# Optimization experiments

Hardware: AMD Instinct MI355X
Metric: run time of the kernel (lower is better)

## Reference

```python
import jax, jax.numpy as jnp
from jax import lax
import numpy as np

B, T, IN, H, OUT = 1024, 512, 64, 128, 2
BN_EPS = 1e-5


def _gru_layer(x, w_ih, w_hh, b_ih, b_hh):
    # x: [B, T, F]; w_ih: [3H, F]; w_hh: [3H, H]; gate order = (r, z, n) as in PyTorch
    Bb = x.shape[0]
    Hh = w_hh.shape[1]
    xg = jnp.einsum('btf,gf->btg', x, w_ih) + b_ih  # precompute input gates [B, T, 3H]

    def step(h, xg_t):
        hg = h @ w_hh.T + b_hh                       # [B, 3H]
        xr, xz, xn = jnp.split(xg_t, 3, axis=-1)
        hr, hz, hn = jnp.split(hg, 3, axis=-1)
        r = jax.nn.sigmoid(xr + hr)
        z = jax.nn.sigmoid(xz + hz)
        n = jnp.tanh(xn + r * hn)
        h_new = (1.0 - z) * n + z * h
        return h_new, h_new

    h0 = jnp.zeros((Bb, Hh), dtype=x.dtype)
    _, ys = lax.scan(step, h0, jnp.swapaxes(xg, 0, 1))  # scan over time
    return jnp.swapaxes(ys, 0, 1)                        # [B, T, H]


def setup_inputs() -> dict:
    key = jax.random.key(0)
    ks = jax.random.split(key, 16)
    s_in = 1.0 / np.sqrt(H)  # PyTorch GRU init scale
    d = {
        'x': jax.random.normal(ks[0], (B, T, IN), dtype=jnp.float32),
        'w_ih0': jax.random.uniform(ks[1], (3 * H, IN), minval=-s_in, maxval=s_in),
        'w_hh0': jax.random.uniform(ks[2], (3 * H, H), minval=-s_in, maxval=s_in),
        'b_ih0': jax.random.uniform(ks[3], (3 * H,), minval=-s_in, maxval=s_in),
        'b_hh0': jax.random.uniform(ks[4], (3 * H,), minval=-s_in, maxval=s_in),
        'w_ih1': jax.random.uniform(ks[5], (3 * H, H), minval=-s_in, maxval=s_in),
        'w_hh1': jax.random.uniform(ks[6], (3 * H, H), minval=-s_in, maxval=s_in),
        'b_ih1': jax.random.uniform(ks[7], (3 * H,), minval=-s_in, maxval=s_in),
        'b_hh1': jax.random.uniform(ks[8], (3 * H,), minval=-s_in, maxval=s_in),
        'fc1_w': jax.random.normal(ks[9], (H // 2, H)) * 0.05,
        'fc1_b': jnp.zeros((H // 2,)),
        'fc2_w': jax.random.normal(ks[10], (OUT, H // 2)) * 0.05,
        'fc2_b': jnp.zeros((OUT,)),
        'bn_gamma': jnp.ones((H // 2,)),
        'bn_beta': jnp.zeros((H // 2,)),
        'bn_mean': jnp.zeros((H // 2,)),
        'bn_var': jnp.ones((H // 2,)),
    }
    return d


def reference(x, w_ih0, w_hh0, b_ih0, b_hh0, w_ih1, w_hh1, b_ih1, b_hh1,
              fc1_w, fc1_b, fc2_w, fc2_b, bn_gamma, bn_beta, bn_mean, bn_var):
    h1 = _gru_layer(x, w_ih0, w_hh0, b_ih0, b_hh0)   # [B, T, H]
    h2 = _gru_layer(h1, w_ih1, w_hh1, b_ih1, b_hh1)  # [B, T, H]
    out = h2[:, -1, :]                                # last timestep [B, H]
    # dropout = identity (eval mode)
    out = jax.nn.relu(out @ fc1_w.T + fc1_b)          # [B, H/2]
    out = (out - bn_mean) * jax.lax.rsqrt(bn_var + BN_EPS) * bn_gamma + bn_beta
    out = out @ fc2_w.T + fc2_b                       # [B, 2]
    return out
```

## Files before the change

kernel.cpp:

```cpp
#include <hip/hip_runtime.h>
#include <hip/hip_bf16.h>

namespace {

typedef _Float16 h16;
typedef _Float16 f16x8 __attribute__((ext_vector_type(8)));
typedef _Float16 f16x4 __attribute__((ext_vector_type(4)));
typedef _Float16 f16x2 __attribute__((ext_vector_type(2)));
typedef float    f32x4 __attribute__((ext_vector_type(4)));

constexpr int T_SEQ = 512;
constexpr int B_SZ  = 1024;
constexpr int H_DIM = 128;
constexpr int ROWS  = 16;
constexpr int NT    = 512;
constexpr int KSH   = 4;
constexpr int KSX0  = 2;
constexpr int KSX1  = 4;
constexpr int ROWP0 = 192 + 8;
constexpr int ROWP1 = 256 + 8;

__global__ __launch_bounds__(NT, 1)
void gru2(const float* __restrict__ x,
          const float* __restrict__ w_ih0,
          const float* __restrict__ w_hh0,
          const float* __restrict__ b_ih0, const float* __restrict__ b_hh0,
          const float* __restrict__ w_ih1,
          const float* __restrict__ w_hh1,
          const float* __restrict__ b_ih1, const float* __restrict__ b_hh1,
          float* __restrict__ h2out)
{
  __shared__ __align__(16) h16 hx0[2][ROWS][ROWP0];
  __shared__ __align__(16) h16 hx1[2][ROWS][ROWP1];

  const int tid = threadIdx.x;
  const int wv  = tid >> 6;
  const int ln  = tid & 63;
  const int q   = ln >> 4;
  const int lr  = ln & 15;
  const int r0  = blockIdx.x * ROWS;
  const int j0  = wv * 16 + q * 4;

  auto ldw = [](const float* pw) {
    const float4 v0 = *(const float4*)(pw);
    const float4 v1 = *(const float4*)(pw + 4);
    f16x8 f;
    f[0]=(h16)v0.x; f[1]=(h16)v0.y; f[2]=(h16)v0.z; f[3]=(h16)v0.w;
    f[4]=(h16)v1.x; f[5]=(h16)v1.y; f[6]=(h16)v1.z; f[7]=(h16)v1.w;
    return f;
  };

  f16x8 wA0[3][KSH], wB0[3][KSX0], wA1[3][KSH], wB1[3][KSX1];
  #pragma unroll
  for (int p = 0; p < 3; ++p) {
    const int g = p * H_DIM + wv * 16 + lr;
    #pragma unroll
    for (int ks = 0; ks < KSH; ++ks) {
      wA0[p][ks] = ldw(w_hh0 + (size_t)g * H_DIM + ks * 32 + q * 8);
      wA1[p][ks] = ldw(w_hh1 + (size_t)g * H_DIM + ks * 32 + q * 8);
    }
    #pragma unroll
    for (int ks = 0; ks < KSX0; ++ks)
      wB0[p][ks] = ldw(w_ih0 + (size_t)g * 64 + ks * 32 + q * 8);
    #pragma unroll
    for (int ks = 0; ks < KSX1; ++ks)
      wB1[p][ks] = ldw(w_ih1 + (size_t)g * H_DIM + ks * 32 + q * 8);
  }

  f32x4 bR0, bZ0, bNx0, bNh0, bR1, bZ1, bNx1, bNh1;
  {
    auto mkb = [&](const float* bi, const float* bh,
                   f32x4& bR, f32x4& bZ, f32x4& bNx, f32x4& bNh) {
      const float4 ir  = *(const float4*)&bi[j0];
      const float4 hr  = *(const float4*)&bh[j0];
      const float4 iz  = *(const float4*)&bi[H_DIM + j0];
      const float4 hz  = *(const float4*)&bh[H_DIM + j0];
      const float4 in_ = *(const float4*)&bi[2 * H_DIM + j0];
      const float4 hn  = *(const float4*)&bh[2 * H_DIM + j0];
      bR[0]=ir.x+hr.x; bR[1]=ir.y+hr.y; bR[2]=ir.z+hr.z; bR[3]=ir.w+hr.w;
      bZ[0]=iz.x+hz.x; bZ[1]=iz.y+hz.y; bZ[2]=iz.z+hz.z; bZ[3]=iz.w+hz.w;
      bNx[0]=in_.x; bNx[1]=in_.y; bNx[2]=in_.z; bNx[3]=in_.w;
      bNh[0]=hn.x;  bNh[1]=hn.y;  bNh[2]=hn.z;  bNh[3]=hn.w;
    };
    mkb(b_ih0, b_hh0, bR0, bZ0, bNx0, bNh0);
    mkb(b_ih1, b_hh1, bR1, bZ1, bNx1, bNh1);
  }

  const int sr = tid >> 5;
  const int si = tid & 31;

  {
    f16x4 z; z[0]=z[1]=z[2]=z[3] = (h16)0.f;
    *(f16x4*)&hx0[0][tid >> 5][(tid & 31) * 4] = z;
    *(f16x4*)&hx1[1][tid >> 5][(tid & 31) * 4] = z;
  }
  {
    const float2 v = *(const float2*)(x + ((size_t)(r0 + sr) * T_SEQ + 0) * 64 + si * 2);
    f16x2 s0; s0[0] = (h16)v.x; s0[1] = (h16)v.y;
    *(f16x2*)&hx0[0][sr][H_DIM + si * 2] = s0;
  }
  f16x2 sA, sB;
  {
    const float2 v = *(const float2*)(x + ((size_t)(r0 + sr) * T_SEQ + 1) * 64 + si * 2);
    sA[0] = (h16)v.x; sA[1] = (h16)v.y;
  }
  f16x4 h_old0, h_old1;
  h_old0[0]=h_old0[1]=h_old0[2]=h_old0[3] = (h16)0.f;
  h_old1 = h_old0;
  __syncthreads();

  auto gates = [&](const f32x4& aR, const f32x4& aZ, const f32x4& aNx, const f32x4& aNh,
                   f16x4& h_old, float* hnv) -> f16x4 {
    f16x4 nv4;
    #pragma unroll
    for (int i = 0; i < 4; ++i) {
      const float rg = __builtin_amdgcn_rcpf(1.f + __expf(-aR[i]));
      const float zg = __builtin_amdgcn_rcpf(1.f + __expf(-aZ[i]));
      const float na = aNx[i] + rg * aNh[i];
      const float e2 = __expf(2.f * na);
      const float ng = 1.f - 2.f * __builtin_amdgcn_rcpf(e2 + 1.f);
      const float ho = (float)h_old[i];
      const float hn = ng + zg * (ho - ng);
      hnv[i] = hn;
      nv4[i] = (h16)hn;
    }
    h_old = nv4;
    return nv4;
  };

  auto l0_step = [&](int g, int cur, f16x2& s_use, f16x2& s_load) {
    f16x8 bh[KSH], bx[KSX0];
    #pragma unroll
    for (int ks = 0; ks < KSH; ++ks)
      bh[ks] = *(const f16x8*)&hx0[cur][lr][ks * 32 + q * 8];
    #pragma unroll
    for (int ks = 0; ks < KSX0; ++ks)
      bx[ks] = *(const f16x8*)&hx0[cur][lr][H_DIM + ks * 32 + q * 8];

    {
      const int tt = (g + 2 < T_SEQ) ? g + 2 : T_SEQ - 1;
      const float2 v = *(const float2*)(x + ((size_t)(r0 + sr) * T_SEQ + tt) * 64 + si * 2);
      s_load[0] = (h16)v.x; s_load[1] = (h16)v.y;
    }

    f32x4 aR = bR0, aZ = bZ0, aNh = bNh0, aNx = bNx0;
    #pragma unroll
    for (int ks = 0; ks < KSH; ++ks) {
      aR  = __builtin_amdgcn_mfma_f32_16x16x32_f16(wA0[0][ks], bh[ks], aR, 0, 0, 0);
      aZ  = __builtin_amdgcn_mfma_f32_16x16x32_f16(wA0[1][ks], bh[ks], aZ, 0, 0, 0);
      aNh = __builtin_amdgcn_mfma_f32_16x16x32_f16(wA0[2][ks], bh[ks], aNh, 0, 0, 0);
    }
    #pragma unroll
    for (int ks = 0; ks < KSX0; ++ks) {
      aR  = __builtin_amdgcn_mfma_f32_16x16x32_f16(wB0[0][ks], bx[ks], aR, 0, 0, 0);
      aZ  = __builtin_amdgcn_mfma_f32_16x16x32_f16(wB0[1][ks], bx[ks], aZ, 0, 0, 0);
      aNx = __builtin_amdgcn_mfma_f32_16x16x32_f16(wB0[2][ks], bx[ks], aNx, 0, 0, 0);
    }

    float hnv[4];
    const f16x4 nv4 = gates(aR, aZ, aNx, aNh, h_old0, hnv);
    *(f16x4*)&hx0[cur ^ 1][lr][j0] = nv4;
    *(f16x4*)&hx1[cur ^ 1][lr][H_DIM + j0] = nv4;
    *(f16x2*)&hx0[cur ^ 1][sr][H_DIM + si * 2] = s_use;
  };

  auto l1_step = [&](int cur, bool final_store) {
    f16x8 bh[KSH], bx[KSX1];
    #pragma unroll
    for (int ks = 0; ks < KSH; ++ks)
      bh[ks] = *(const f16x8*)&hx1[cur][lr][ks * 32 + q * 8];
    #pragma unroll
    for (int ks = 0; ks < KSX1; ++ks)
      bx[ks] = *(const f16x8*)&hx1[cur][lr][H_DIM + ks * 32 + q * 8];

    f32x4 aR = bR1, aZ = bZ1, aNh = bNh1, aNx = bNx1;
    #pragma unroll
    for (int ks = 0; ks < KSH; ++ks) {
      aR  = __builtin_amdgcn_mfma_f32_16x16x32_f16(wA1[0][ks], bh[ks], aR, 0, 0, 0);
      aZ  = __builtin_amdgcn_mfma_f32_16x16x32_f16(wA1[1][ks], bh[ks], aZ, 0, 0, 0);
      aNh = __builtin_amdgcn_mfma_f32_16x16x32_f16(wA1[2][ks], bh[ks], aNh, 0, 0, 0);
    }
    #pragma unroll
    for (int ks = 0; ks < KSX1; ++ks) {
      aR  = __builtin_amdgcn_mfma_f32_16x16x32_f16(wB1[0][ks], bx[ks], aR, 0, 0, 0);
      aZ  = __builtin_amdgcn_mfma_f32_16x16x32_f16(wB1[1][ks], bx[ks], aZ, 0, 0, 0);
      aNx = __builtin_amdgcn_mfma_f32_16x16x32_f16(wB1[2][ks], bx[ks], aNx, 0, 0, 0);
    }

    float hnv[4];
    const f16x4 nv4 = gates(aR, aZ, aNx, aNh, h_old1, hnv);
    *(f16x4*)&hx1[cur ^ 1][lr][j0] = nv4;
    if (final_store)
      *(float4*)&h2out[(size_t)(r0 + lr) * H_DIM + j0] =
          make_float4(hnv[0], hnv[1], hnv[2], hnv[3]);
  };

  l0_step(0, 0, sA, sB);
  __syncthreads();

  #pragma unroll 1
  for (int k = 0; k < (T_SEQ - 2) / 2; ++k) {
    l0_step(2 * k + 1, 1, sB, sA);
    l1_step(1, false);
    __syncthreads();
    l0_step(2 * k + 2, 0, sA, sB);
    l1_step(0, false);
    __syncthreads();
  }
  l0_step(T_SEQ - 1, 1, sB, sA);
  l1_step(1, false);
  __syncthreads();
  l1_step(0, true);
}

__global__ __launch_bounds__(64)
void head_kernel(const float* __restrict__ h2,
                 const float* __restrict__ fc1_w, const float* __restrict__ fc1_b,
                 const float* __restrict__ fc2_w, const float* __restrict__ fc2_b,
                 const float* __restrict__ gamma, const float* __restrict__ beta,
                 const float* __restrict__ mean,  const float* __restrict__ var,
                 float* __restrict__ out)
{
  const int row = blockIdx.x;
  const int j   = threadIdx.x;
  __shared__ __align__(16) float hrow[H_DIM];
  __shared__ __align__(16) float act[64];

  hrow[j]      = h2[(size_t)row * H_DIM + j];
  hrow[64 + j] = h2[(size_t)row * H_DIM + 64 + j];
  __syncthreads();

  float s = fc1_b[j];
  const float4* wr = reinterpret_cast<const float4*>(fc1_w + (size_t)j * H_DIM);
  #pragma unroll
  for (int k4 = 0; k4 < H_DIM / 4; ++k4) {
    const float4 w = wr[k4];
    const float4 h = reinterpret_cast<const float4*>(hrow)[k4];
    s += w.x * h.x + w.y * h.y + w.z * h.z + w.w * h.w;
  }
  s = fmaxf(s, 0.f);
  s = (s - mean[j]) * rsqrtf(var[j] + 1e-5f) * gamma[j] + beta[j];
  act[j] = s;
  __syncthreads();

  if (j < 2) {
    float o = fc2_b[j];
    #pragma unroll
    for (int k = 0; k < 64; ++k) o += fc2_w[(size_t)j * 64 + k] * act[k];
    out[(size_t)row * 2 + j] = o;
  }
}

}

extern "C" void kernel_launch(void* const* d_in, const int* in_sizes, int n_in,
                              void* d_out, int out_size, void* d_ws, size_t ws_size,
                              hipStream_t stream) {
  const float* x     = (const float*)d_in[0];
  const float* w_ih0 = (const float*)d_in[1];
  const float* w_hh0 = (const float*)d_in[2];
  const float* b_ih0 = (const float*)d_in[3];
  const float* b_hh0 = (const float*)d_in[4];
  const float* w_ih1 = (const float*)d_in[5];
  const float* w_hh1 = (const float*)d_in[6];
  const float* b_ih1 = (const float*)d_in[7];
  const float* b_hh1 = (const float*)d_in[8];
  const float* fc1_w = (const float*)d_in[9];
  const float* fc1_b = (const float*)d_in[10];
  const float* fc2_w = (const float*)d_in[11];
  const float* fc2_b = (const float*)d_in[12];
  const float* gamma = (const float*)d_in[13];
  const float* beta  = (const float*)d_in[14];
  const float* mean  = (const float*)d_in[15];
  const float* var   = (const float*)d_in[16];
  float* out = (float*)d_out;

  const size_t h2_bytes = (size_t)B_SZ * H_DIM * sizeof(float);
  if (ws_size < h2_bytes) return;
  float* h2 = (float*)d_ws;

  gru2<<<dim3(B_SZ / ROWS), dim3(NT), 0, stream>>>(
      x, w_ih0, w_hh0, b_ih0, b_hh0, w_ih1, w_hh1, b_ih1, b_hh1, h2);
  head_kernel<<<dim3(B_SZ), dim3(64), 0, stream>>>(
      h2, fc1_w, fc1_b, fc2_w, fc2_b, gamma, beta, mean, var, out);
}
```

Baseline: 702.0 us.

## Reuse layer-0 hidden fragments for layer-1 input gates and swizzle LDS layout

Layer 1's input-gate projection is now computed inside the layer-0 step, reusing the h1 fragments already loaded for layer 0's recurrent matmul, instead of separately reading h1 from a concatenated layer-1 buffer. The LDS buffers are repacked into a fragment-major slot layout so each lane reads one contiguous 16-byte chunk (ln-indexed), which is meant to avoid bank conflicts and padding. The x staging switches to 8-wide vector loads done by two waves. This lowers the LDS reads and writes per step but holds the layer-1 input gates in registers across the barrier, raising register pressure.

```diff
diff --git a/kernel.cpp b/kernel.cpp
--- a/kernel.cpp
+++ b/kernel.cpp
@@ -6,7 +6,6 @@
 typedef _Float16 h16;
 typedef _Float16 f16x8 __attribute__((ext_vector_type(8)));
 typedef _Float16 f16x4 __attribute__((ext_vector_type(4)));
-typedef _Float16 f16x2 __attribute__((ext_vector_type(2)));
 typedef float    f32x4 __attribute__((ext_vector_type(4)));
 
 constexpr int T_SEQ = 512;
@@ -14,11 +13,13 @@
 constexpr int H_DIM = 128;
 constexpr int ROWS  = 16;
 constexpr int NT    = 512;
-constexpr int KSH   = 4;
-constexpr int KSX0  = 2;
-constexpr int KSX1  = 4;
-constexpr int ROWP0 = 192 + 8;
-constexpr int ROWP1 = 256 + 8;
+constexpr int CH    = 4;
+constexpr int CX    = 2;
+
+constexpr int FH1 = 0;
+constexpr int FX  = 2 * CH * 64;
+constexpr int FH2 = FX + 2 * CX * 64;
+constexpr int NSLOT = FH2 + 2 * CH * 64;
 
 __global__ __launch_bounds__(NT, 1)
 void gru2(const float* __restrict__ x,
@@ -30,8 +31,7 @@
           const float* __restrict__ b_ih1, const float* __restrict__ b_hh1,
           float* __restrict__ h2out)
 {
-  __shared__ __align__(16) h16 hx0[2][ROWS][ROWP0];
-  __shared__ __align__(16) h16 hx1[2][ROWS][ROWP1];
+  __shared__ __align__(16) h16 lds[NSLOT * 8];
 
   const int tid = threadIdx.x;
   const int wv  = tid >> 6;
@@ -41,6 +41,9 @@
   const int r0  = blockIdx.x * ROWS;
   const int j0  = wv * 16 + q * 4;
 
+  const int slotH = (wv >> 1) * 64 + ((wv & 1) * 2 + (q >> 1)) * 16 + lr;
+  const int e0    = (q & 1) * 4;
+
   auto ldw = [](const float* pw) {
     const float4 v0 = *(const float4*)(pw);
     const float4 v1 = *(const float4*)(pw + 4);
@@ -50,21 +53,19 @@
     return f;
   };
 
-  f16x8 wA0[3][KSH], wB0[3][KSX0], wA1[3][KSH], wB1[3][KSX1];
+  f16x8 wA0[3][CH], wB0[3][CX], wI1[3][CH], wA1[3][CH];
   #pragma unroll
   for (int p = 0; p < 3; ++p) {
     const int g = p * H_DIM + wv * 16 + lr;
     #pragma unroll
-    for (int ks = 0; ks < KSH; ++ks) {
+    for (int ks = 0; ks < CH; ++ks) {
       wA0[p][ks] = ldw(w_hh0 + (size_t)g * H_DIM + ks * 32 + q * 8);
+      wI1[p][ks] = ldw(w_ih1 + (size_t)g * H_DIM + ks * 32 + q * 8);
       wA1[p][ks] = ldw(w_hh1 + (size_t)g * H_DIM + ks * 32 + q * 8);
     }
     #pragma unroll
-    for (int ks = 0; ks < KSX0; ++ks)
+    for (int ks = 0; ks < CX; ++ks)
       wB0[p][ks] = ldw(w_ih0 + (size_t)g * 64 + ks * 32 + q * 8);
-    #pragma unroll
-    for (int ks = 0; ks < KSX1; ++ks)
-      wB1[p][ks] = ldw(w_ih1 + (size_t)g * H_DIM + ks * 32 + q * 8);
   }
 
   f32x4 bR0, bZ0, bNx0, bNh0, bR1, bZ1, bNx1, bNh1;
@@ -86,31 +87,45 @@
     mkb(b_ih1, b_hh1, bR1, bZ1, bNx1, bNh1);
   }
 
-  const int sr = tid >> 5;
-  const int si = tid & 31;
-
-  {
-    f16x4 z; z[0]=z[1]=z[2]=z[3] = (h16)0.f;
-    *(f16x4*)&hx0[0][tid >> 5][(tid & 31) * 4] = z;
-    *(f16x4*)&hx1[1][tid >> 5][(tid & 31) * 4] = z;
-  }
-  {
-    const float2 v = *(const float2*)(x + ((size_t)(r0 + sr) * T_SEQ + 0) * 64 + si * 2);
-    f16x2 s0; s0[0] = (h16)v.x; s0[1] = (h16)v.y;
-    *(f16x2*)&hx0[0][sr][H_DIM + si * 2] = s0;
-  }
-  f16x2 sA, sB;
-  {
-    const float2 v = *(const float2*)(x + ((size_t)(r0 + sr) * T_SEQ + 1) * 64 + si * 2);
-    sA[0] = (h16)v.x; sA[1] = (h16)v.y;
-  }
+  const int  sc  = tid >> 6;
+  const int  sl  = tid & 63;
+  const bool stg = (tid < CX * 64);
+  const size_t xrow = (size_t)(r0 + (sl & 15)) * T_SEQ;
+  const int    xk   = (sl >> 4) * 8 + sc * 32;
+
+  auto load_x = [&](int t, f16x8& d) {
+    if (stg) {
+      const float* p = x + (xrow + t) * 64 + xk;
+      const float4 v0 = *(const float4*)(p);
+      const float4 v1 = *(const float4*)(p + 4);
+      d[0]=(h16)v0.x; d[1]=(h16)v0.y; d[2]=(h16)v0.z; d[3]=(h16)v0.w;
+      d[4]=(h16)v1.x; d[5]=(h16)v1.y; d[6]=(h16)v1.z; d[7]=(h16)v1.w;
+    }
+  };
+  auto stage_x = [&](int buf, const f16x8& s) {
+    if (stg) *(f16x8*)&lds[(FX + buf * CX * 64 + sc * 64 + sl) * 8] = s;
+  };
+  auto rd = [&](int cb) {
+    return *(const f16x8*)&lds[(cb + ln) * 8];
+  };
+
+  {
+    f16x8 z; z[0]=z[1]=z[2]=z[3]=z[4]=z[5]=z[6]=z[7] = (h16)0.f;
+    if (tid < 256) *(f16x8*)&lds[(FH1 + tid) * 8] = z;
+    else           *(f16x8*)&lds[(FH2 + 256 + (tid - 256)) * 8] = z;
+  }
+  f16x8 s0; load_x(0, s0); stage_x(0, s0);
+  f16x8 sA; load_x(1, sA);
+  f16x8 sB;
   f16x4 h_old0, h_old1;
   h_old0[0]=h_old0[1]=h_old0[2]=h_old0[3] = (h16)0.f;
   h_old1 = h_old0;
   __syncthreads();
 
-  auto gates = [&](const f32x4& aR, const f32x4& aZ, const f32x4& aNx, const f32x4& aNh,
-                   f16x4& h_old, float* hnv) -> f16x4 {
+  f32x4 xR, xZ, xN;
+
+  auto gates = [&](const f32x4& aR, const f32x4& aZ, const f32x4& aNx,
+                   const f32x4& aNh, f16x4& h_old, float* hnv) -> f16x4 {
     f16x4 nv4;
     #pragma unroll
     for (int i = 0; i < 4; ++i) {
@@ -128,89 +143,107 @@
     return nv4;
   };
 
-  auto l0_step = [&](int g, int cur, f16x2& s_use, f16x2& s_load) {
-    f16x8 bh[KSH], bx[KSX0];
-    #pragma unroll
-    for (int ks = 0; ks < KSH; ++ks)
-      bh[ks] = *(const f16x8*)&hx0[cur][lr][ks * 32 + q * 8];
-    #pragma unroll
-    for (int ks = 0; ks < KSX0; ++ks)
-      bx[ks] = *(const f16x8*)&hx0[cur][lr][H_DIM + ks * 32 + q * 8];
-
-    {
-      const int tt = (g + 2 < T_SEQ) ? g + 2 : T_SEQ - 1;
-      const float2 v = *(const float2*)(x + ((size_t)(r0 + sr) * T_SEQ + tt) * 64 + si * 2);
-      s_load[0] = (h16)v.x; s_load[1] = (h16)v.y;
-    }
+  auto xg_calc = [&](const f16x8* bh) {
+    xR = bR1; xZ = bZ1; xN = bNx1;
+    #pragma unroll
+    for (int ks = 0; ks < CH; ++ks) {
+      xR = __builtin_amdgcn_mfma_f32_16x16x32_f16(wI1[0][ks], bh[ks], xR, 0, 0, 0);
+      xZ = __builtin_amdgcn_mfma_f32_16x16x32_f16(wI1[1][ks], bh[ks], xZ, 0, 0, 0);
+      xN = __builtin_amdgcn_mfma_f32_16x16x32_f16(wI1[2][ks], bh[ks], xN, 0, 0, 0);
+    }
+  };
+
+  auto l0_step = [&](int g, int cur, f16x8& s_use, f16x8& s_load, const f16x8* bh) {
+    f16x8 bx[CX];
+    #pragma unroll
+    for (int c = 0; c < CX; ++c) bx[c] = rd(FX + cur * CX * 64 + c * 64);
+
+    load_x((g + 2 < T_SEQ) ? g + 2 : T_SEQ - 1, s_load);
 
     f32x4 aR = bR0, aZ = bZ0, aNh = bNh0, aNx = bNx0;
     #pragma unroll
-    for (int ks = 0; ks < KSH; ++ks) {
+    for (int ks = 0; ks < CH; ++ks) {
       aR  = __builtin_amdgcn_mfma_f32_16x16x32_f16(wA0[0][ks], bh[ks], aR, 0, 0, 0);
       aZ  = __builtin_amdgcn_mfma_f32_16x16x32_f16(wA0[1][ks], bh[ks], aZ, 0, 0, 0);
       aNh = __builtin_amdgcn_mfma_f32_16x16x32_f16(wA0[2][ks], bh[ks], aNh, 0, 0, 0);
     }
     #pragma unroll
-    for (int ks = 0; ks < KSX0; ++ks) {
-      aR  = __builtin_amdgcn_mfma_f32_16x16x32_f16(wB0[0][ks], bx[ks], aR, 0, 0, 0);
-      aZ  = __builtin_amdgcn_mfma_f32_16x16x32_f16(wB0[1][ks], bx[ks], aZ, 0, 0, 0);
-      aNx = __builtin_amdgcn_mfma_f32_16x16x32_f16(wB0[2][ks], bx[ks], aNx, 0, 0, 0);
-    }
+    for (int c = 0; c < CX; ++c) {
+      aR  = __builtin_amdgcn_mfma_f32_16x16x32_f16(wB0[0][c], bx[c], aR, 0, 0, 0);
+      aZ  = __builtin_amdgcn_mfma_f32_16x16x32_f16(wB0[1][c], bx[c], aZ, 0, 0, 0);
+      aNx = __builtin_amdgcn_mfma_f32_16x16x32_f16(wB0[2][c], bx[c], aNx, 0, 0, 0);
+    }
+    xg_calc(bh);
 
     float hnv[4];
     const f16x4 nv4 = gates(aR, aZ, aNx, aNh, h_old0, hnv);
-    *(f16x4*)&hx0[cur ^ 1][lr][j0] = nv4;
-    *(f16x4*)&hx1[cur ^ 1][lr][H_DIM + j0] = nv4;
-    *(f16x2*)&hx0[cur ^ 1][sr][H_DIM + si * 2] = s_use;
-  };
-
-  auto l1_step = [&](int cur, bool final_store) {
-    f16x8 bh[KSH], bx[KSX1];
-    #pragma unroll
-    for (int ks = 0; ks < KSH; ++ks)
-      bh[ks] = *(const f16x8*)&hx1[cur][lr][ks * 32 + q * 8];
-    #pragma unroll
-    for (int ks = 0; ks < KSX1; ++ks)
-      bx[ks] = *(const f16x8*)&hx1[cur][lr][H_DIM + ks * 32 + q * 8];
-
-    f32x4 aR = bR1, aZ = bZ1, aNh = bNh1, aNx = bNx1;
-    #pragma unroll
-    for (int ks = 0; ks < KSH; ++ks) {
-      aR  = __builtin_amdgcn_mfma_f32_16x16x32_f16(wA1[0][ks], bh[ks], aR, 0, 0, 0);
-      aZ  = __builtin_amdgcn_mfma_f32_16x16x32_f16(wA1[1][ks], bh[ks], aZ, 0, 0, 0);
-      aNh = __builtin_amdgcn_mfma_f32_16x16x32_f16(wA1[2][ks], bh[ks], aNh, 0, 0, 0);
-    }
-    #pragma unroll
-    for (int ks = 0; ks < KSX1; ++ks) {
-      aR  = __builtin_amdgcn_mfma_f32_16x16x32_f16(wB1[0][ks], bx[ks], aR, 0, 0, 0);
-      aZ  = __builtin_amdgcn_mfma_f32_16x16x32_f16(wB1[1][ks], bx[ks], aZ, 0, 0, 0);
-      aNx = __builtin_amdgcn_mfma_f32_16x16x32_f16(wB1[2][ks], bx[ks], aNx, 0, 0, 0);
-    }
-
+    *(f16x4*)&lds[(FH1 + (cur ^ 1) * 256 + slotH) * 8 + e0] = nv4;
+    stage_x(cur ^ 1, s_use);
+  };
+
+  auto l1_step = [&](int cur, bool fin) {
+    f16x8 bh2[CH];
+    #pragma unroll
+    for (int ks = 0; ks < CH; ++ks) bh2[ks] = rd(FH2 + cur * 256 + ks * 64);
+
+    f32x4 aR = xR, aZ = xZ, aNh = bNh1;
+    #pragma unroll
+    for (int ks = 0; ks < CH; ++ks) {
+      aR  = __builtin_amdgcn_mfma_f32_16x16x32_f16(wA1[0][ks], bh2[ks], aR, 0, 0, 0);
+      aZ  = __builtin_amdgcn_mfma_f32_16x16x32_f16(wA1[1][ks], bh2[ks], aZ, 0, 0, 0);
+      aNh = __builtin_amdgcn_mfma_f32_16x16x32_f16(wA1[2][ks], bh2[ks], aNh, 0, 0, 0);
+    }
     float hnv[4];
-    const f16x4 nv4 = gates(aR, aZ, aNx, aNh, h_old1, hnv);
-    *(f16x4*)&hx1[cur ^ 1][lr][j0] = nv4;
-    if (final_store)
+    const f16x4 nv4 = gates(aR, aZ, xN, aNh, h_old1, hnv);
+    *(f16x4*)&lds[(FH2 + (cur ^ 1) * 256 + slotH) * 8 + e0] = nv4;
+    if (fin)
       *(float4*)&h2out[(size_t)(r0 + lr) * H_DIM + j0] =
           make_float4(hnv[0], hnv[1], hnv[2], hnv[3]);
   };
 
-  l0_step(0, 0, sA, sB);
+  {
+    f16x8 bh[CH];
+    #pragma unroll
+    for (int ks = 0; ks < CH; ++ks) bh[ks] = rd(FH1 + 0 + ks * 64);
+    l0_step(0, 0, sA, sB, bh);
+  }
+  __syncthreads();
+  {
+    f16x8 bh[CH];
+    #pragma unroll
+    for (int ks = 0; ks < CH; ++ks) bh[ks] = rd(FH1 + 256 + ks * 64);
+    l0_step(1, 1, sB, sA, bh);
+    l1_step(1, false);
+  }
   __syncthreads();
 
   #pragma unroll 1
-  for (int k = 0; k < (T_SEQ - 2) / 2; ++k) {
-    l0_step(2 * k + 1, 1, sB, sA);
-    l1_step(1, false);
+  for (int k = 1; k <= 255; ++k) {
+    {
+      f16x8 bh[CH];
+      #pragma unroll
+      for (int ks = 0; ks < CH; ++ks) bh[ks] = rd(FH1 + 0 + ks * 64);
+      l0_step(2 * k, 0, sA, sB, bh);
+      l1_step(0, false);
+    }
     __syncthreads();
-    l0_step(2 * k + 2, 0, sA, sB);
-    l1_step(0, false);
+    {
+      f16x8 bh[CH];
+      #pragma unroll
+      for (int ks = 0; ks < CH; ++ks) bh[ks] = rd(FH1 + 256 + ks * 64);
+      l0_step(2 * k + 1, 1, sB, sA, bh);
+      l1_step(1, false);
+    }
     __syncthreads();
   }
-  l0_step(T_SEQ - 1, 1, sB, sA);
-  l1_step(1, false);
-  __syncthreads();
-  l1_step(0, true);
+
+  {
+    f16x8 bh[CH];
+    #pragma unroll
+    for (int ks = 0; ks < CH; ++ks) bh[ks] = rd(FH1 + 0 + ks * 64);
+    xg_calc(bh);
+    l1_step(0, true);
+  }
 }
 
 __global__ __launch_bounds__(64)
```

New measurement: 919.9 us. +31.0%, slower.
